# Performance work log

Hardware: AMD Instinct MI355X
Metric: run time of the kernel (lower is better)

Reference implementation:

```python
import jax, jax.numpy as jnp
import numpy as np

B, S, D, F = 8, 2048, 256, 8

def setup_inputs() -> dict:
    key = jax.random.key(0)
    ks = jax.random.split(key, 7)
    hidden_states = jax.random.normal(ks[0], (B, S, D), dtype=jnp.float32)
    # flat indices into zero-prepended [1 + B*S, D] token table; 0 = padding row
    select_idx = jax.random.randint(ks[1], (B, S, F), 0, B * S + 1, dtype=jnp.int32)
    word_mask = jax.random.randint(ks[2], (B, S), 0, 2, dtype=jnp.int32)
    W1 = jax.random.normal(ks[3], (D, D), dtype=jnp.float32) * (1.0 / np.sqrt(D))
    b1 = jax.random.normal(ks[4], (D,), dtype=jnp.float32) * 0.02
    w2 = jax.random.normal(ks[5], (D,), dtype=jnp.float32) * (1.0 / np.sqrt(D))
    b2 = jax.random.normal(ks[6], (1,), dtype=jnp.float32) * 0.02
    return {"hidden_states": hidden_states, "select_idx": select_idx,
            "word_mask": word_mask, "W1": W1, "b1": b1, "w2": w2, "b2": b2}

def reference(hidden_states, select_idx, word_mask, W1, b1, w2, b2):
    b, s, d = hidden_states.shape
    h = jnp.tanh(hidden_states.reshape(-1, d) @ W1.T + b1)          # [B*S, D]
    h = jnp.concatenate([jnp.zeros((1, d), h.dtype), h], axis=0)    # zero padding row at index 0
    g = h[select_idx.reshape(-1)]                                    # gather: [B*S*F, D]
    g = g.reshape(b * s, -1, d).max(axis=1)                          # AdaptiveMaxPool1d(1) over word occurrences
    scores = (g @ w2 + b2[0]).reshape(b, s)                          # w2 linear -> [B, S]
    neg = -10000.0 * (1.0 - word_mask.astype(jnp.float32))
    return scores.astype(jnp.float32) + neg
```

## Files before the change

### kernel.cpp

```cpp
#include <hip/hip_runtime.h>
#include <hip/hip_bf16.h>
#include <math.h>

#define BB 8
#define SS 2048
#define DD 256
#define FF 8
#define NTOK (BB*SS)

typedef __bf16 bf16x8 __attribute__((ext_vector_type(8)));
typedef float  f32x4  __attribute__((ext_vector_type(4)));
typedef float  f32x2  __attribute__((ext_vector_type(2)));

#define BM 64
#define CH 64
#define NCH (DD/CH)

__device__ __forceinline__ float fast_tanh(float x) {
    float e = __expf(2.0f * x);
    return 1.0f - 2.0f * __builtin_amdgcn_rcpf(e + 1.0f);
}

__device__ __forceinline__ unsigned pack2_bf16(float a, float b) {
    return (__float_as_uint(a) >> 16) | (__float_as_uint(b) & 0xFFFF0000u);
}

__device__ __forceinline__ unsigned char f32_to_fp8(float v) {
    return (unsigned char)(__builtin_amdgcn_cvt_pk_fp8_f32(v, v, 0, false) & 0xFF);
}

__global__ __launch_bounds__(512, 2) void gemm_tanh_kernel(
    const float* __restrict__ x, const float* __restrict__ W1,
    const float* __restrict__ b1, unsigned char* __restrict__ table)
{
    __shared__ __align__(16) unsigned short wt[2][CH * DD];

    const int tid  = threadIdx.x;
    const int bx   = blockIdx.x;
    const int tok0 = bx * BM;

    if (bx == 0 && tid < 64) ((unsigned int*)table)[tid] = 0u;

    const int wave = tid >> 6, lane = tid & 63;
    const int wm = wave >> 1;
    const int wn = wave & 1;
    const int lr = lane & 15;
    const int kg = lane >> 4;

    const float* xrow = x + (size_t)(tok0 + wm * 16 + lr) * DD + kg * 8;
    f32x4 xa[8], xb[8];
    #pragma unroll
    for (int c = 0; c < 8; ++c) {
        xa[c] = *(const f32x4*)&xrow[c * 32];
        xb[c] = *(const f32x4*)&xrow[c * 32 + 4];
    }

    const int srow = tid >> 3;
    const int scol = (tid & 7) * 32;
    f32x4 wr0[8], wrn[8];

    auto wload = [&](int nc, f32x4* wr) {
        const float* wsrc = W1 + (size_t)(nc * CH + srow) * DD + scol;
        #pragma unroll
        for (int j = 0; j < 8; ++j) wr[j] = *(const f32x4*)&wsrc[j * 4];
    };
    auto wstore = [&](int buf, const f32x4* wr) {
        #pragma unroll
        for (int j = 0; j < 4; ++j) {
            uint4 p;
            p.x = pack2_bf16(wr[2*j].x,   wr[2*j].y);
            p.y = pack2_bf16(wr[2*j].z,   wr[2*j].w);
            p.z = pack2_bf16(wr[2*j+1].x, wr[2*j+1].y);
            p.w = pack2_bf16(wr[2*j+1].z, wr[2*j+1].w);
            int q  = (scol >> 3) + j;
            int qp = q ^ (srow & 7);
            *(uint4*)&wt[buf][srow * DD + qp * 8] = p;
        }
    };

    wload(0, wr0);

    bf16x8 af[8];
    #pragma unroll
    for (int c = 0; c < 8; ++c) {
        uint4 p;
        p.x = pack2_bf16(xa[c].x, xa[c].y);
        p.y = pack2_bf16(xa[c].z, xa[c].w);
        p.z = pack2_bf16(xb[c].x, xb[c].y);
        p.w = pack2_bf16(xb[c].z, xb[c].w);
        af[c] = *(bf16x8*)&p;
    }

    wstore(0, wr0);
    __syncthreads();

    f32x4 acc[NCH][2];
    #pragma unroll
    for (int nc = 0; nc < NCH; ++nc)
        #pragma unroll
        for (int nf = 0; nf < 2; ++nf)
            acc[nc][nf] = (f32x4){0.f, 0.f, 0.f, 0.f};

    const int nl0 = wn * 32 + lr;
    const int nl1 = nl0 + 16;
    const int sw  = lr & 7;

    #pragma unroll
    for (int nc = 0; nc < NCH; ++nc) {
        const int buf = nc & 1;
        if (nc + 1 < NCH) wload(nc + 1, wrn);

        #pragma unroll
        for (int c = 0; c < 8; ++c) {
            int q  = c * 4 + kg;
            int qp = q ^ sw;
            bf16x8 bf0 = *(const bf16x8*)&wt[buf][nl0 * DD + qp * 8];
            bf16x8 bf1 = *(const bf16x8*)&wt[buf][nl1 * DD + qp * 8];
            acc[nc][0] = __builtin_amdgcn_mfma_f32_16x16x32_bf16(af[c], bf0, acc[nc][0], 0, 0, 0);
            acc[nc][1] = __builtin_amdgcn_mfma_f32_16x16x32_bf16(af[c], bf1, acc[nc][1], 0, 0, 0);
        }

        if (nc + 1 < NCH) {
            wstore(buf ^ 1, wrn);
            __syncthreads();
        }
    }

    float bj[NCH][2];
    #pragma unroll
    for (int nc = 0; nc < NCH; ++nc) {
        bj[nc][0] = b1[nc * CH + wn * 32 + lr];
        bj[nc][1] = b1[nc * CH + wn * 32 + 16 + lr];
    }

    unsigned char* sc = (unsigned char*)&wt[0][0];
    #pragma unroll
    for (int nc = 0; nc < NCH; ++nc) {
        #pragma unroll
        for (int nf = 0; nf < 2; ++nf) {
            #pragma unroll
            for (int r = 0; r < 4; ++r) {
                int row = wm * 16 + kg * 4 + r;
                int col = nc * CH + wn * 32 + nf * 16 + lr;
                float v = fast_tanh(acc[nc][nf][r] + bj[nc][nf]);
                sc[row * 272 + col] = f32_to_fp8(v);
            }
        }
    }
    __syncthreads();
    {
        int row = tid >> 3;
        int off = (tid & 7) * 32;
        uint4 v0 = *(const uint4*)&sc[row * 272 + off];
        uint4 v1 = *(const uint4*)&sc[row * 272 + off + 16];
        *(uint4*)&table[(size_t)(1 + tok0 + row) * DD + off]      = v0;
        *(uint4*)&table[(size_t)(1 + tok0 + row) * DD + off + 16] = v1;
    }
}

__global__ __launch_bounds__(256) void gather_score_kernel(
    const unsigned char* __restrict__ table,
    const int* __restrict__ select_idx,
    const int* __restrict__ word_mask,
    const float* __restrict__ w2,
    const float* __restrict__ b2,
    float* __restrict__ out)
{
    const int tid  = threadIdx.x;
    const int lane = tid & 63;
    const int wv   = tid >> 6;
    const int i    = blockIdx.x * 4 + wv;
    const int half = lane >> 5;
    const int c    = lane & 31;
    const int d0   = c * 8;

    const int4* sp = (const int4*)(select_idx + (size_t)i * FF);
    int4 q0 = sp[0], q1 = sp[1];
    int rows[4];
    rows[0] = half ? q0.y : q0.x;
    rows[1] = half ? q0.w : q0.z;
    rows[2] = half ? q1.y : q1.x;
    rows[3] = half ? q1.w : q1.z;

    float m[8];
    #pragma unroll
    for (int j = 0; j < 8; ++j) m[j] = -INFINITY;

    #pragma unroll
    for (int it = 0; it < 4; ++it) {
        uint2 u = *(const uint2*)(table + (size_t)rows[it] * DD + d0);
        f32x2 a0 = __builtin_amdgcn_cvt_pk_f32_fp8(u.x, false);
        f32x2 a1 = __builtin_amdgcn_cvt_pk_f32_fp8(u.x, true);
        f32x2 a2 = __builtin_amdgcn_cvt_pk_f32_fp8(u.y, false);
        f32x2 a3 = __builtin_amdgcn_cvt_pk_f32_fp8(u.y, true);
        m[0] = fmaxf(m[0], a0.x); m[1] = fmaxf(m[1], a0.y);
        m[2] = fmaxf(m[2], a1.x); m[3] = fmaxf(m[3], a1.y);
        m[4] = fmaxf(m[4], a2.x); m[5] = fmaxf(m[5], a2.y);
        m[6] = fmaxf(m[6], a3.x); m[7] = fmaxf(m[7], a3.y);
    }

    #pragma unroll
    for (int j = 0; j < 8; ++j) m[j] = fmaxf(m[j], __shfl_xor(m[j], 32));

    f32x4 wa = *(const f32x4*)&w2[d0];
    f32x4 wb = *(const f32x4*)&w2[d0 + 4];
    float p = m[0] * wa.x + m[1] * wa.y + m[2] * wa.z + m[3] * wa.w
            + m[4] * wb.x + m[5] * wb.y + m[6] * wb.z + m[7] * wb.w;

    #pragma unroll
    for (int off = 16; off; off >>= 1) p += __shfl_xor(p, off);

    if (lane == 0) {
        float neg = word_mask[i] ? 0.f : -10000.f;
        out[i] = p + b2[0] + neg;
    }
}

extern "C" void kernel_launch(void* const* d_in, const int* in_sizes, int n_in,
                              void* d_out, int out_size, void* d_ws, size_t ws_size,
                              hipStream_t stream) {
    const float* hs    = (const float*)d_in[0];
    const int*   sidx  = (const int*)  d_in[1];
    const int*   wmask = (const int*)  d_in[2];
    const float* W1    = (const float*)d_in[3];
    const float* b1    = (const float*)d_in[4];
    const float* w2    = (const float*)d_in[5];
    const float* b2    = (const float*)d_in[6];
    float* out = (float*)d_out;

    unsigned char* table = (unsigned char*)d_ws;

    gemm_tanh_kernel<<<NTOK / BM, 512, 0, stream>>>(hs, W1, b1, table);
    gather_score_kernel<<<NTOK / 4, 256, 0, stream>>>(table, sidx, wmask, w2, b2, out);
}
```

Baseline: 96.88 us.

## Pre-convert W1 to bf16 and stream it from global with smaller token tiles

Adds a small kernel that converts W1 to bf16 once per call into workspace. The GEMM kernel then stages a 32-token x tile in LDS and has each wave read its bf16 W1 fragments straight from global/L2, instead of converting and double-buffering W1 through LDS in every block. BM drops from 64 to 32 and occupancy is raised to 4 blocks per CU. This removes per-block W1 conversion and LDS staging and the barriers between chunks, but adds a kernel launch and relies on L2 hits for the W1 reloads across blocks.

```diff
diff --git a/kernel.cpp b/kernel.cpp
--- a/kernel.cpp
+++ b/kernel.cpp
@@ -12,28 +12,38 @@
 typedef float  f32x4  __attribute__((ext_vector_type(4)));
 typedef float  f32x2  __attribute__((ext_vector_type(2)));
 
-#define BM 64
-#define CH 64
-#define NCH (DD/CH)
+__device__ __forceinline__ unsigned pack2_bf16(float a, float b) {
+    return (__float_as_uint(a) >> 16) | (__float_as_uint(b) & 0xFFFF0000u);
+}
+
+__global__ __launch_bounds__(256) void w1_to_bf16_kernel(
+    const float* __restrict__ W1, unsigned short* __restrict__ W1b)
+{
+    int i = blockIdx.x * 256 + threadIdx.x;
+    f32x4 a = *(const f32x4*)&W1[(size_t)i * 8];
+    f32x4 b = *(const f32x4*)&W1[(size_t)i * 8 + 4];
+    uint4 p;
+    p.x = pack2_bf16(a.x, a.y); p.y = pack2_bf16(a.z, a.w);
+    p.z = pack2_bf16(b.x, b.y); p.w = pack2_bf16(b.z, b.w);
+    *(uint4*)&W1b[(size_t)i * 8] = p;
+}
+
+#define BM 32
 
 __device__ __forceinline__ float fast_tanh(float x) {
     float e = __expf(2.0f * x);
     return 1.0f - 2.0f * __builtin_amdgcn_rcpf(e + 1.0f);
 }
 
-__device__ __forceinline__ unsigned pack2_bf16(float a, float b) {
-    return (__float_as_uint(a) >> 16) | (__float_as_uint(b) & 0xFFFF0000u);
-}
-
 __device__ __forceinline__ unsigned char f32_to_fp8(float v) {
     return (unsigned char)(__builtin_amdgcn_cvt_pk_fp8_f32(v, v, 0, false) & 0xFF);
 }
 
-__global__ __launch_bounds__(512, 2) void gemm_tanh_kernel(
-    const float* __restrict__ x, const float* __restrict__ W1,
+__global__ __launch_bounds__(512, 4) void gemm_tanh_kernel(
+    const float* __restrict__ x, const unsigned short* __restrict__ W1b,
     const float* __restrict__ b1, unsigned char* __restrict__ table)
 {
-    __shared__ __align__(16) unsigned short wt[2][CH * DD];
+    __shared__ __align__(16) unsigned short xs[BM * DD];
 
     const int tid  = threadIdx.x;
     const int bx   = blockIdx.x;
@@ -42,119 +52,73 @@
     if (bx == 0 && tid < 64) ((unsigned int*)table)[tid] = 0u;
 
     const int wave = tid >> 6, lane = tid & 63;
-    const int wm = wave >> 1;
-    const int wn = wave & 1;
+    const int n0 = wave * 32;
     const int lr = lane & 15;
     const int kg = lane >> 4;
 
-    const float* xrow = x + (size_t)(tok0 + wm * 16 + lr) * DD + kg * 8;
-    f32x4 xa[8], xb[8];
-    #pragma unroll
-    for (int c = 0; c < 8; ++c) {
-        xa[c] = *(const f32x4*)&xrow[c * 32];
-        xb[c] = *(const f32x4*)&xrow[c * 32 + 4];
-    }
-
-    const int srow = tid >> 3;
-    const int scol = (tid & 7) * 32;
-    f32x4 wr0[8], wrn[8];
-
-    auto wload = [&](int nc, f32x4* wr) {
-        const float* wsrc = W1 + (size_t)(nc * CH + srow) * DD + scol;
-        #pragma unroll
-        for (int j = 0; j < 8; ++j) wr[j] = *(const f32x4*)&wsrc[j * 4];
-    };
-    auto wstore = [&](int buf, const f32x4* wr) {
-        #pragma unroll
-        for (int j = 0; j < 4; ++j) {
-            uint4 p;
-            p.x = pack2_bf16(wr[2*j].x,   wr[2*j].y);
-            p.y = pack2_bf16(wr[2*j].z,   wr[2*j].w);
-            p.z = pack2_bf16(wr[2*j+1].x, wr[2*j+1].y);
-            p.w = pack2_bf16(wr[2*j+1].z, wr[2*j+1].w);
-            int q  = (scol >> 3) + j;
-            int qp = q ^ (srow & 7);
-            *(uint4*)&wt[buf][srow * DD + qp * 8] = p;
-        }
-    };
-
-    wload(0, wr0);
-
-    bf16x8 af[8];
-    #pragma unroll
-    for (int c = 0; c < 8; ++c) {
-        uint4 p;
-        p.x = pack2_bf16(xa[c].x, xa[c].y);
-        p.y = pack2_bf16(xa[c].z, xa[c].w);
-        p.z = pack2_bf16(xb[c].x, xb[c].y);
-        p.w = pack2_bf16(xb[c].z, xb[c].w);
-        af[c] = *(bf16x8*)&p;
-    }
-
-    wstore(0, wr0);
+    #pragma unroll
+    for (int p = 0; p < 4; ++p) {
+        int s = p * 512 + tid;
+        int row = s >> 6, k4 = s & 63;
+        f32x4 v = *(const f32x4*)&x[(size_t)(tok0 + row) * DD + k4 * 4];
+        uint2 pk;
+        pk.x = pack2_bf16(v.x, v.y);
+        pk.y = pack2_bf16(v.z, v.w);
+        int g  = k4 >> 1;
+        int gp = g ^ (row & 7);
+        *(uint2*)&xs[row * DD + gp * 8 + (k4 & 1) * 4] = pk;
+    }
     __syncthreads();
 
-    f32x4 acc[NCH][2];
-    #pragma unroll
-    for (int nc = 0; nc < NCH; ++nc)
+    f32x4 acc[2][2];
+    #pragma unroll
+    for (int mf = 0; mf < 2; ++mf)
         #pragma unroll
         for (int nf = 0; nf < 2; ++nf)
-            acc[nc][nf] = (f32x4){0.f, 0.f, 0.f, 0.f};
-
-    const int nl0 = wn * 32 + lr;
-    const int nl1 = nl0 + 16;
-    const int sw  = lr & 7;
-
-    #pragma unroll
-    for (int nc = 0; nc < NCH; ++nc) {
-        const int buf = nc & 1;
-        if (nc + 1 < NCH) wload(nc + 1, wrn);
-
-        #pragma unroll
-        for (int c = 0; c < 8; ++c) {
-            int q  = c * 4 + kg;
-            int qp = q ^ sw;
-            bf16x8 bf0 = *(const bf16x8*)&wt[buf][nl0 * DD + qp * 8];
-            bf16x8 bf1 = *(const bf16x8*)&wt[buf][nl1 * DD + qp * 8];
-            acc[nc][0] = __builtin_amdgcn_mfma_f32_16x16x32_bf16(af[c], bf0, acc[nc][0], 0, 0, 0);
-            acc[nc][1] = __builtin_amdgcn_mfma_f32_16x16x32_bf16(af[c], bf1, acc[nc][1], 0, 0, 0);
-        }
-
-        if (nc + 1 < NCH) {
-            wstore(buf ^ 1, wrn);
-            __syncthreads();
-        }
-    }
-
-    float bj[NCH][2];
-    #pragma unroll
-    for (int nc = 0; nc < NCH; ++nc) {
-        bj[nc][0] = b1[nc * CH + wn * 32 + lr];
-        bj[nc][1] = b1[nc * CH + wn * 32 + 16 + lr];
-    }
-
-    unsigned char* sc = (unsigned char*)&wt[0][0];
-    #pragma unroll
-    for (int nc = 0; nc < NCH; ++nc) {
+            acc[mf][nf] = (f32x4){0.f, 0.f, 0.f, 0.f};
+
+    const unsigned short* wrow0 = W1b + (size_t)(n0 + lr) * DD + kg * 8;
+    const unsigned short* wrow1 = W1b + (size_t)(n0 + 16 + lr) * DD + kg * 8;
+    const int sw = lr & 7;
+
+    #pragma unroll
+    for (int c = 0; c < 8; ++c) {
+        int g   = c * 4 + kg;
+        int gp8 = (g ^ sw) * 8;
+        bf16x8 af0 = *(const bf16x8*)&xs[lr * DD + gp8];
+        bf16x8 af1 = *(const bf16x8*)&xs[(16 + lr) * DD + gp8];
+        bf16x8 bf0 = *(const bf16x8*)&wrow0[c * 32];
+        bf16x8 bf1 = *(const bf16x8*)&wrow1[c * 32];
+        acc[0][0] = __builtin_amdgcn_mfma_f32_16x16x32_bf16(af0, bf0, acc[0][0], 0, 0, 0);
+        acc[0][1] = __builtin_amdgcn_mfma_f32_16x16x32_bf16(af0, bf1, acc[0][1], 0, 0, 0);
+        acc[1][0] = __builtin_amdgcn_mfma_f32_16x16x32_bf16(af1, bf0, acc[1][0], 0, 0, 0);
+        acc[1][1] = __builtin_amdgcn_mfma_f32_16x16x32_bf16(af1, bf1, acc[1][1], 0, 0, 0);
+    }
+
+    float bj0 = b1[n0 + lr];
+    float bj1 = b1[n0 + 16 + lr];
+
+    __syncthreads();
+    unsigned char* sc = (unsigned char*)&xs[0];
+    #pragma unroll
+    for (int mf = 0; mf < 2; ++mf) {
         #pragma unroll
         for (int nf = 0; nf < 2; ++nf) {
             #pragma unroll
             for (int r = 0; r < 4; ++r) {
-                int row = wm * 16 + kg * 4 + r;
-                int col = nc * CH + wn * 32 + nf * 16 + lr;
-                float v = fast_tanh(acc[nc][nf][r] + bj[nc][nf]);
+                int row = mf * 16 + kg * 4 + r;
+                int col = n0 + nf * 16 + lr;
+                float v = fast_tanh(acc[mf][nf][r] + (nf ? bj1 : bj0));
                 sc[row * 272 + col] = f32_to_fp8(v);
             }
         }
     }
     __syncthreads();
     {
-        int row = tid >> 3;
-        int off = (tid & 7) * 32;
-        uint4 v0 = *(const uint4*)&sc[row * 272 + off];
-        uint4 v1 = *(const uint4*)&sc[row * 272 + off + 16];
-        *(uint4*)&table[(size_t)(1 + tok0 + row) * DD + off]      = v0;
-        *(uint4*)&table[(size_t)(1 + tok0 + row) * DD + off + 16] = v1;
+        int row = tid >> 4;
+        int off = (tid & 15) * 16;
+        uint4 v = *(const uint4*)&sc[row * 272 + off];
+        *(uint4*)&table[(size_t)(1 + tok0 + row) * DD + off] = v;
     }
 }
 
@@ -228,8 +192,10 @@
     const float* b2    = (const float*)d_in[6];
     float* out = (float*)d_out;
 
-    unsigned char* table = (unsigned char*)d_ws;
-
-    gemm_tanh_kernel<<<NTOK / BM, 512, 0, stream>>>(hs, W1, b1, table);
+    unsigned char*  table = (unsigned char*)d_ws;
+    unsigned short* W1b   = (unsigned short*)((char*)d_ws + (8u << 20));
+
+    w1_to_bf16_kernel<<<32, 256, 0, stream>>>(W1, W1b);
+    gemm_tanh_kernel<<<NTOK / BM, 512, 0, stream>>>(hs, W1b, b1, table);
     gather_score_kernel<<<NTOK / 4, 256, 0, stream>>>(table, sidx, wmask, w2, b2, out);
 }
```

Measured after the change: 90.46 us. 1.07x faster.
